# Kernel tuning notes

Hardware: AMD Instinct MI355X
Metric: run time of the kernel (lower is better)

The kernel has to match this reference:

```python
import jax, jax.numpy as jnp
import numpy as np

CLIP = 100000.0

def heaviside(x):
    # smooth Heaviside approximation
    return (jnp.tanh(5.0 * x) + 1.0) / 2.0

def snowbucket(s0, t, ddf, tmax):
    ddf = ddf * 5.0
    tmax = tmax * 3.0
    return heaviside(t - tmax) * heaviside(s0) * jnp.minimum(s0, ddf * (t - tmax))

def soilbucket(s1, pet, f, smax, qmax, k):
    k = k / 10.0
    f = f / 10.0
    smax = smax * 1500.0
    qmax = qmax * 50.0
    h_pos = heaviside(s1)
    h_over = heaviside(s1 - smax)
    h_under = heaviside(smax - s1)
    et = h_pos * h_over * pet + h_pos * h_under * pet * (s1 / smax)
    qsub = h_pos * h_over * qmax + h_pos * h_under * qmax * jnp.exp(-f * (smax - s1))
    qsurf = h_pos * h_over * (s1 - smax)
    qst = qsub * k
    qgr = qsub * (1.0 - k)
    return et, qsurf, qst, qgr

def setup_inputs() -> dict:
    key = jax.random.key(0)
    ks = jax.random.split(key, 8)
    B, T = 8192, 1024
    prcp = jax.random.uniform(ks[0], (B, T, 1), jnp.float32) * 10.0   # mm/day
    tmean = jax.random.uniform(ks[1], (B, T, 1), jnp.float32) * 30.0 - 5.0  # deg C
    dayl = jax.random.uniform(ks[2], (B, T, 1), jnp.float32) * 0.5 + 0.25   # day fraction
    inputs = jnp.concatenate([prcp, tmean, dayl], axis=-1)
    def p(i):
        return jax.random.uniform(ks[i], (1,), jnp.float32) * 0.6 + 0.2
    return {"inputs": inputs, "f": p(3), "smax": p(4), "qmax": p(5),
            "ddf": p(6), "tmin": p(7), "tmax": p(3), "k": p(4)}

def reference(inputs, f, smax, qmax, ddf, tmin, tmax, k):
    # inputs: (B, T, 3) = [prcp, tmean, dayl]
    prcp = inputs[:, :, 0]
    tmean = inputs[:, :, 1]
    dayl = inputs[:, :, 2]
    pet = 29.8 * (dayl * 24.0) * 0.611 * jnp.exp(17.3 * tmean / (tmean + 237.3)) / (tmean + 273.2)

    tmin_s = tmin * -3.0

    # scan over time: carry = (s0, s1) each (B,)
    xs = jnp.stack([prcp, tmean, pet], axis=-1).transpose(1, 0, 2)  # (T, B, 3)

    def step(carry, x):
        s0, s1 = carry
        p_, t_, pet_ = x[:, 0], x[:, 1], x[:, 2]
        psnow = heaviside(tmin_s - t_) * p_
        prain = heaviside(t_ - tmin_s) * p_
        m = snowbucket(s0, t_, ddf, tmax)
        et, qsurf, qst, qgr = soilbucket(s1, pet_, f, smax, qmax, k)
        ds0 = psnow - m
        ds1 = prain + m - et - qsurf - qst - qgr
        ns0 = s0 + jnp.clip(ds0, -CLIP, CLIP)
        ns1 = s1 + jnp.clip(ds1, -CLIP, CLIP)
        return (ns0, ns1), (ns0, ns1)

    B = inputs.shape[0]
    init = (jnp.zeros((B,), inputs.dtype), jnp.zeros((B,), inputs.dtype))
    _, (s0_seq, s1_seq) = jax.lax.scan(step, init, xs)
    s0_seq = s0_seq.T  # (B, T)
    s1_seq = s1_seq.T

    # post-hoc flux computation on state sequences (as in call())
    _m = snowbucket(s0_seq, tmean, ddf, tmax)
    et, qsurf, qst, qgr = soilbucket(s1_seq, pet, f, smax, qmax, k)
    # mode == 'normal': note original names qsurf 'qsub' and outputs qsub+qst
    return jnp.stack([qsurf + qst, qgr], axis=-1)  # (B, T, 2)
```

## Files before the change

### kernel.cpp

```cpp
#include <hip/hip_runtime.h>

#define CLIPV 100000.0f
typedef __attribute__((address_space(3))) void as3void;
typedef __attribute__((address_space(1))) void as1void;

__device__ __forceinline__ float fexp2(float x){ return __builtin_amdgcn_exp2f(x); }
__device__ __forceinline__ float frcp(float x){ return __builtin_amdgcn_rcpf(x); }

#define WAIT_VM(N) { asm volatile("s_waitcnt vmcnt(" #N ")" ::: "memory"); \
                     __builtin_amdgcn_sched_barrier(0); }
#define LGKM0_BAR() { asm volatile("s_waitcnt lgkmcnt(0)" ::: "memory"); \
                      __builtin_amdgcn_s_barrier(); }

extern "C" __global__ void __launch_bounds__(128)
prnn_kernel(const float* __restrict__ inp,
            const float* __restrict__ fpar,  const float* __restrict__ smaxp,
            const float* __restrict__ qmaxp, const float* __restrict__ ddfp,
            const float* __restrict__ tminp, const float* __restrict__ tmaxp,
            const float* __restrict__ kp,
            float* __restrict__ out)
{
    __shared__ alignas(16) unsigned char lin[2][13312];
    __shared__ alignas(16) float prodb[2][16 * 64 * 6];
    __shared__ alignas(16) float lcons[2][16 * 65 * 2];

    const int tid = threadIdx.x;
    const int l   = tid & 63;
    const int wv  = tid >> 6;
    const int c0  = blockIdx.x * 64;

    const float NL = -14.426950408889634f;
    float f10    = fpar[0] * 0.1f;
    float smax_s = smaxp[0] * 1500.0f;
    float qmax_s = qmaxp[0] * 50.0f;
    float ddf5   = ddfp[0] * 5.0f;
    float tmin_s = tminp[0] * -3.0f;
    float tmax3  = tmaxp[0] * 3.0f;
    float k10    = kp[0] * 0.1f;
    float inv_smax = 1.0f / smax_s;
    float cw     = 14.426950408889634f * tmin_s;
    float Kc     = fexp2(14.426950408889634f * (tmax3 - tmin_s));
    float cf     = 1.4426950408889634f * f10;

    const float* gin  = inp + (size_t)c0 * 3072;
    float*       gout = out + (size_t)c0 * 2048;

    if (wv == 1) {
        auto stage_load = [&](int s, int pb) {
            const float* gb = gin + s * 48;
            #pragma unroll
            for (int k2 = 0; k2 < 13; ++k2) {
                unsigned e = (unsigned)(k2 * 64 + l);
                unsigned r = (e * 161321u) >> 21;
                int q = (int)(e - r * 13u);
                q = (q > 11) ? 11 : q;
                const float* g = gb + r * 3072 + q * 4;
                __builtin_amdgcn_global_load_lds((as1void*)g,
                    (as3void*)(&lin[pb][k2 * 1024]), 16, 0, 0);
            }
        };

        auto prod_step = [&](float* pw, int u, float p, float tm, float dl) {
            float t1 = tm + 237.3f, t2 = tm + 273.2f;
            float r12 = frcp(t1 * t2);
            float e1  = fexp2(24.958624207f * tm * (r12 * t2));
            float pet = 436.9872f * dl * e1 * (r12 * t1);
            float ew  = fexp2(fmaf(NL, tm, cw));
            float w   = frcp(1.0f + ew);
            float prain = w * p;
            float psnow = p - prain;
            float eg1 = 1.0f + fminf(ew * Kc, 1e30f);
            float tmg = ddf5 * (tm - tmax3);
            float* o = pw + u * 384 + l * 6;
            *(float2*)(o)     = make_float2(prain, psnow);
            *(float2*)(o + 2) = make_float2(pet, eg1);
            o[4] = tmg;
        };

        auto prod_compute = [&](int s) {
            const unsigned char* myrow = &lin[s & 1][l * 208];
            float* pw = prodb[s & 1];
            #pragma unroll
            for (int u4 = 0; u4 < 4; ++u4) {
                float4 A = *(const float4*)(myrow + u4 * 48);
                float4 B = *(const float4*)(myrow + u4 * 48 + 16);
                float4 C = *(const float4*)(myrow + u4 * 48 + 32);
                prod_step(pw, u4 * 4 + 0, A.x, A.y, A.z);
                prod_step(pw, u4 * 4 + 1, A.w, B.x, B.y);
                prod_step(pw, u4 * 4 + 2, B.z, B.w, C.x);
                prod_step(pw, u4 * 4 + 3, C.y, C.z, C.w);
            }
        };

        auto writeback = [&](int s) {
            float* gb = gout + s * 32;
            const float* lc = lcons[s & 1];
            #pragma unroll
            for (int k2 = 0; k2 < 9; ++k2) {
                unsigned e = (unsigned)(k2 * 64 + l);
                unsigned r = (e * 233017u) >> 21;
                int q = (int)(e - r * 9u);
                if (q < 8) {
                    const float* p0 = lc + (2 * q) * 130 + r * 2;
                    float2 a = *(const float2*)(p0);
                    float2 b = *(const float2*)(p0 + 130);
                    float aqst = a.y * k10, bqst = b.y * k10;
                    float4 v = make_float4(a.x + aqst, a.y - aqst,
                                           b.x + bqst, b.y - bqst);
                    *(float4*)(gb + r * 2048 + q * 4) = v;
                }
            }
        };

        stage_load(0, 0);
        WAIT_VM(0);
        stage_load(1, 1);
        prod_compute(0);
        LGKM0_BAR();
        stage_load(2, 0);
        WAIT_VM(13);
        prod_compute(1);
        LGKM0_BAR();
        for (int i = 2; i <= 62; ++i) {
            writeback(i - 2);
            stage_load(i + 1, (i + 1) & 1);
            WAIT_VM(22);
            prod_compute(i);
            LGKM0_BAR();
        }
        writeback(61);
        WAIT_VM(9);
        prod_compute(63);
        LGKM0_BAR();
        writeback(62);
        LGKM0_BAR();
        writeback(63);
    } else {
        float s0v = 0.0f, s1v = 0.0f, qq, c_et;
        {
            float d  = -smax_s;
            float eo = fminf(fexp2(NL * d), 1e30f);
            float ep = 1.0f;
            float hpo = frcp((1.0f + ep) * (1.0f + eo));
            float hpu = eo * hpo;
            float e   = fexp2(cf * d);
            float qsub  = qmax_s * fmaf(hpu, e, hpo);
            float qsurf = hpo * d;
            qq   = qsurf + qsub;
            c_et = fmaf(hpu * 0.0f, inv_smax, hpo);
        }
        LGKM0_BAR();
        for (int i = 1; i <= 64; ++i) {
            const int s = i - 1;
            const float* pr = prodb[s & 1];
            float* lc = lcons[s & 1];
            #pragma unroll
            for (int u = 0; u < 16; ++u) {
                const float* pb = pr + u * 384 + l * 6;
                float2 v0 = *(const float2*)(pb);
                float2 v1 = *(const float2*)(pb + 2);
                float tmg = pb[4];
                float es0 = fexp2(NL * s0v);
                float hg  = frcp((1.0f + es0) * v1.y);
                float m   = hg * fminf(s0v, tmg);
                float et  = c_et * v1.x;
                float ds0 = v0.y - m;
                float ds1 = v0.x + m - et - qq;
                s0v += fminf(fmaxf(ds0, -CLIPV), CLIPV);
                s1v += fminf(fmaxf(ds1, -CLIPV), CLIPV);
                float d   = s1v - smax_s;
                float eo  = fminf(fexp2(NL * d), 1e30f);
                float ep  = fminf(fexp2(NL * s1v), 1e30f);
                float hpo = frcp((1.0f + ep) * (1.0f + eo));
                float hpu = eo * hpo;
                float e   = fexp2(cf * d);
                float qsub  = qmax_s * fmaf(hpu, e, hpo);
                float qsurf = hpo * d;
                qq   = qsurf + qsub;
                c_et = fmaf(hpu * s1v, inv_smax, hpo);
                *(float2*)(lc + u * 130 + l * 2) = make_float2(qsurf, qsub);
            }
            LGKM0_BAR();
        }
    }
}

extern "C" void kernel_launch(void* const* d_in, const int* in_sizes, int n_in,
                              void* d_out, int out_size, void* d_ws, size_t ws_size,
                              hipStream_t stream) {
    const float* inp = (const float*)d_in[0];
    const int B = in_sizes[0] / 3072;
    prnn_kernel<<<B / 64, 128, 0, stream>>>(
        inp,
        (const float*)d_in[1],
        (const float*)d_in[2],
        (const float*)d_in[3],
        (const float*)d_in[4],
        (const float*)d_in[5],
        (const float*)d_in[6],
        (const float*)d_in[7],
        (float*)d_out);
}
```

Measured before the change: 308.6 us.

## Restructure LDS handoff to per-lane SoA blocks and simplify scan algebra

Moves the producer and consumer LDS buffers from a timestep-major layout to a per-lane row layout. Each lane now writes and reads 16 timesteps as contiguous float4 vectors, and the consumer preloads its whole block into registers before running the serial recurrence. The recurrence is algebraically simplified: the hg denominator becomes a single fma, and qq, c_et and the stored outputs are computed with fewer multiplies. Writeback is adjusted so it emits qsurf+qst and qgr from the stored qq and qsub. The aim is to cut LDS instruction count and latency on the serial critical path, at the cost of more registers and a padded stride that may cause bank conflicts.

```diff
diff --git a/kernel.cpp b/kernel.cpp
--- a/kernel.cpp
+++ b/kernel.cpp
@@ -12,7 +12,7 @@
 #define LGKM0_BAR() { asm volatile("s_waitcnt lgkmcnt(0)" ::: "memory"); \
                       __builtin_amdgcn_s_barrier(); }
 
-extern "C" __global__ void __launch_bounds__(128)
+extern "C" __global__ void __launch_bounds__(128, 1)
 prnn_kernel(const float* __restrict__ inp,
             const float* __restrict__ fpar,  const float* __restrict__ smaxp,
             const float* __restrict__ qmaxp, const float* __restrict__ ddfp,
@@ -21,8 +21,8 @@
             float* __restrict__ out)
 {
     __shared__ alignas(16) unsigned char lin[2][13312];
-    __shared__ alignas(16) float prodb[2][16 * 64 * 6];
-    __shared__ alignas(16) float lcons[2][16 * 65 * 2];
+    __shared__ alignas(16) float prodb[2][64 * 84];
+    __shared__ alignas(16) float lcons[2][64 * 36];
 
     const int tid = threadIdx.x;
     const int l   = tid & 63;
@@ -37,10 +37,11 @@
     float tmin_s = tminp[0] * -3.0f;
     float tmax3  = tmaxp[0] * 3.0f;
     float k10    = kp[0] * 0.1f;
-    float inv_smax = 1.0f / smax_s;
+    float ism    = 1.0f / smax_s;
     float cw     = 14.426950408889634f * tmin_s;
     float Kc     = fexp2(14.426950408889634f * (tmax3 - tmin_s));
     float cf     = 1.4426950408889634f * f10;
+    float k1m    = 1.0f - k10;
 
     const float* gin  = inp + (size_t)c0 * 3072;
     float*       gout = out + (size_t)c0 * 2048;
@@ -60,35 +61,38 @@
             }
         };
 
-        auto prod_step = [&](float* pw, int u, float p, float tm, float dl) {
+        auto prod_one = [&](float p, float tm, float dl,
+                            float& pr, float& ps, float& pe, float& eg, float& tg) {
             float t1 = tm + 237.3f, t2 = tm + 273.2f;
             float r12 = frcp(t1 * t2);
             float e1  = fexp2(24.958624207f * tm * (r12 * t2));
-            float pet = 436.9872f * dl * e1 * (r12 * t1);
-            float ew  = fexp2(fmaf(NL, tm, cw));
-            float w   = frcp(1.0f + ew);
-            float prain = w * p;
-            float psnow = p - prain;
-            float eg1 = 1.0f + fminf(ew * Kc, 1e30f);
-            float tmg = ddf5 * (tm - tmax3);
-            float* o = pw + u * 384 + l * 6;
-            *(float2*)(o)     = make_float2(prain, psnow);
-            *(float2*)(o + 2) = make_float2(pet, eg1);
-            o[4] = tmg;
+            pe = 436.9872f * dl * e1 * (r12 * t1);
+            float ew = fexp2(fmaf(NL, tm, cw));
+            float w  = frcp(1.0f + ew);
+            pr = w * p;
+            ps = p - pr;
+            eg = 1.0f + fminf(ew * Kc, 1e30f);
+            tg = ddf5 * (tm - tmax3);
         };
 
         auto prod_compute = [&](int s) {
             const unsigned char* myrow = &lin[s & 1][l * 208];
-            float* pw = prodb[s & 1];
+            float* o = prodb[s & 1] + l * 84;
             #pragma unroll
             for (int u4 = 0; u4 < 4; ++u4) {
                 float4 A = *(const float4*)(myrow + u4 * 48);
                 float4 B = *(const float4*)(myrow + u4 * 48 + 16);
                 float4 C = *(const float4*)(myrow + u4 * 48 + 32);
-                prod_step(pw, u4 * 4 + 0, A.x, A.y, A.z);
-                prod_step(pw, u4 * 4 + 1, A.w, B.x, B.y);
-                prod_step(pw, u4 * 4 + 2, B.z, B.w, C.x);
-                prod_step(pw, u4 * 4 + 3, C.y, C.z, C.w);
+                float pr[4], ps[4], pe[4], eg[4], tg[4];
+                prod_one(A.x, A.y, A.z, pr[0], ps[0], pe[0], eg[0], tg[0]);
+                prod_one(A.w, B.x, B.y, pr[1], ps[1], pe[1], eg[1], tg[1]);
+                prod_one(B.z, B.w, C.x, pr[2], ps[2], pe[2], eg[2], tg[2]);
+                prod_one(C.y, C.z, C.w, pr[3], ps[3], pe[3], eg[3], tg[3]);
+                *(float4*)(o +      u4 * 4) = make_float4(pr[0], pr[1], pr[2], pr[3]);
+                *(float4*)(o + 16 + u4 * 4) = make_float4(ps[0], ps[1], ps[2], ps[3]);
+                *(float4*)(o + 32 + u4 * 4) = make_float4(pe[0], pe[1], pe[2], pe[3]);
+                *(float4*)(o + 48 + u4 * 4) = make_float4(eg[0], eg[1], eg[2], eg[3]);
+                *(float4*)(o + 64 + u4 * 4) = make_float4(tg[0], tg[1], tg[2], tg[3]);
             }
         };
 
@@ -101,12 +105,11 @@
                 unsigned r = (e * 233017u) >> 21;
                 int q = (int)(e - r * 9u);
                 if (q < 8) {
-                    const float* p0 = lc + (2 * q) * 130 + r * 2;
-                    float2 a = *(const float2*)(p0);
-                    float2 b = *(const float2*)(p0 + 130);
-                    float aqst = a.y * k10, bqst = b.y * k10;
-                    float4 v = make_float4(a.x + aqst, a.y - aqst,
-                                           b.x + bqst, b.y - bqst);
+                    const float* p0 = lc + r * 36 + 2 * q;
+                    float2 qqv = *(const float2*)(p0);
+                    float2 qbv = *(const float2*)(p0 + 16);
+                    float o1a = k1m * qbv.x, o1b = k1m * qbv.y;
+                    float4 v = make_float4(qqv.x - o1a, o1a, qqv.y - o1b, o1b);
                     *(float4*)(gb + r * 2048 + q * 4) = v;
                 }
             }
@@ -138,47 +141,64 @@
     } else {
         float s0v = 0.0f, s1v = 0.0f, qq, c_et;
         {
-            float d  = -smax_s;
-            float eo = fminf(fexp2(NL * d), 1e30f);
-            float ep = 1.0f;
-            float hpo = frcp((1.0f + ep) * (1.0f + eo));
-            float hpu = eo * hpo;
+            float d   = -smax_s;
+            float eo  = fminf(fexp2(NL * d), 1e30f);
+            float ep  = 1.0f;
+            float den = (1.0f + ep) * (1.0f + eo);
+            float hpo = frcp(den);
             float e   = fexp2(cf * d);
-            float qsub  = qmax_s * fmaf(hpu, e, hpo);
-            float qsurf = hpo * d;
-            qq   = qsurf + qsub;
-            c_et = fmaf(hpu * 0.0f, inv_smax, hpo);
+            float w1  = fmaf(e, eo, 1.0f);
+            qq   = hpo * fmaf(qmax_s, w1, d);
+            c_et = hpo;
         }
         LGKM0_BAR();
+
         for (int i = 1; i <= 64; ++i) {
-            const int s = i - 1;
-            const float* pr = prodb[s & 1];
-            float* lc = lcons[s & 1];
-            #pragma unroll
-            for (int u = 0; u < 16; ++u) {
-                const float* pb = pr + u * 384 + l * 6;
-                float2 v0 = *(const float2*)(pb);
-                float2 v1 = *(const float2*)(pb + 2);
-                float tmg = pb[4];
+            const int sb = (i - 1) & 1;
+            const float* base = prodb[sb] + l * 84;
+            float4 PR[5][4];
+            #pragma unroll
+            for (int q = 0; q < 5; ++q) {
+                #pragma unroll
+                for (int g = 0; g < 4; ++g)
+                    PR[q][g] = *(const float4*)(base + q * 16 + g * 4);
+            }
+            float* lcb = lcons[sb] + l * 36;
+
+            auto STEP = [&](float prain, float psnow, float pet, float eg1, float tmg,
+                            float& oqq, float& oqb) {
                 float es0 = fexp2(NL * s0v);
-                float hg  = frcp((1.0f + es0) * v1.y);
+                float hg  = frcp(fmaf(es0, eg1, eg1));
                 float m   = hg * fminf(s0v, tmg);
-                float et  = c_et * v1.x;
-                float ds0 = v0.y - m;
-                float ds1 = v0.x + m - et - qq;
+                float ds0 = psnow - m;
                 s0v += fminf(fmaxf(ds0, -CLIPV), CLIPV);
+                float et  = c_et * pet;
+                float pme = (prain + m) - et;
+                float ds1 = pme - qq;
                 s1v += fminf(fmaxf(ds1, -CLIPV), CLIPV);
                 float d   = s1v - smax_s;
                 float eo  = fminf(fexp2(NL * d), 1e30f);
+                float e   = fexp2(cf * d);
                 float ep  = fminf(fexp2(NL * s1v), 1e30f);
-                float hpo = frcp((1.0f + ep) * (1.0f + eo));
-                float hpu = eo * hpo;
-                float e   = fexp2(cf * d);
-                float qsub  = qmax_s * fmaf(hpu, e, hpo);
-                float qsurf = hpo * d;
-                qq   = qsurf + qsub;
-                c_et = fmaf(hpu * s1v, inv_smax, hpo);
-                *(float2*)(lc + u * 130 + l * 2) = make_float2(qsurf, qsub);
+                float den = (1.0f + ep) * (1.0f + eo);
+                float hpo = frcp(den);
+                float w1  = fmaf(e, eo, 1.0f);
+                float qmw = qmax_s * w1;
+                qq   = hpo * (d + qmw);
+                oqb  = hpo * qmw;
+                oqq  = qq;
+                c_et = hpo * fmaf(eo, s1v * ism, 1.0f);
+            };
+
+            #pragma unroll
+            for (int g = 0; g < 4; ++g) {
+                float qs[4], qb[4];
+                STEP(PR[0][g].x, PR[1][g].x, PR[2][g].x, PR[3][g].x, PR[4][g].x, qs[0], qb[0]);
+                STEP(PR[0][g].y, PR[1][g].y, PR[2][g].y, PR[3][g].y, PR[4][g].y, qs[1], qb[1]);
+                STEP(PR[0][g].z, PR[1][g].z, PR[2][g].z, PR[3][g].z, PR[4][g].z, qs[2], qb[2]);
+                STEP(PR[0][g].w, PR[1][g].w, PR[2][g].w, PR[3][g].w, PR[4][g].w, qs[3], qb[3]);
+                *(float4*)(lcb +      g * 4) = make_float4(qs[0], qs[1], qs[2], qs[3]);
+                *(float4*)(lcb + 16 + g * 4) = make_float4(qb[0], qb[1], qb[2], qb[3]);
             }
             LGKM0_BAR();
         }
```

Measured after the change: 304.1 us. Within noise of the previous version (-1.5%).
